# Kernel optimization log

Measured on AMD Instinct MI355X. Metric: run time of the kernel, lower is better.

Reference implementation:

```python
import jax, jax.numpy as jnp
import numpy as np

D_MODEL = 256
D_ENC_M = 256  # mel encoder dim (keys/values), sets temperature = sqrt(D_ENC_M)
D_ENC_T = 256  # text encoder dim (queries)
LN_EPS = 1e-5


def setup_inputs() -> dict:
    key = jax.random.key(0)
    ks = jax.random.split(key, 9)
    B, MEL_LEN, SRC_LEN = 16, 2048, 512
    mel_encoding = jax.random.normal(ks[0], (B, MEL_LEN, D_ENC_M), dtype=jnp.float32)
    text_encoding = jax.random.normal(ks[1], (B, SRC_LEN, D_ENC_T), dtype=jnp.float32)
    mel_mask = jax.random.randint(ks[2], (B, MEL_LEN), 0, 2).astype(bool)
    src_mask = jax.random.randint(ks[3], (B, SRC_LEN), 0, 2).astype(bool)
    # Linear weights (no bias), xavier-uniform style scale
    def xavier(k, shape):
        fan_in, fan_out = shape[1], shape[0]
        lim = jnp.sqrt(6.0 / (fan_in + fan_out))
        return jax.random.uniform(k, shape, jnp.float32, -lim, lim)
    Wq = xavier(ks[4], (D_MODEL, D_ENC_T))
    Wk = xavier(ks[5], (D_MODEL, D_ENC_M))
    Wv = xavier(ks[6], (D_MODEL, D_ENC_M))
    gamma = jnp.ones((D_MODEL,), jnp.float32)
    beta = jnp.zeros((D_MODEL,), jnp.float32)
    return {"mel_encoding": mel_encoding, "text_encoding": text_encoding,
            "mel_mask": mel_mask, "src_mask": src_mask,
            "Wq": Wq, "Wk": Wk, "Wv": Wv, "gamma": gamma, "beta": beta}


def reference(mel_encoding, text_encoding, mel_mask, src_mask, Wq, Wk, Wv, gamma, beta):
    # QKV projections (nn.Linear, bias=False): y = x @ W^T
    q = jnp.einsum('btd,md->btm', text_encoding, Wq)   # [B, src_len, d_model]
    k = jnp.einsum('bsd,md->bsm', mel_encoding, Wk)    # [B, mel_len, d_model]
    v = jnp.einsum('bsd,md->bsm', mel_encoding, Wv)    # [B, mel_len, d_model]
    temperature = jnp.asarray(D_ENC_M, jnp.float32) ** 0.5
    attn = jnp.einsum('btm,bsm->bts', q, k) / temperature  # [B, src_len, mel_len]
    # pre-softmax fill over mel (key) padding
    attn = jnp.where(mel_mask[:, None, :], -jnp.inf, attn)
    attn = jax.nn.softmax(attn, axis=2)
    # post-softmax zeroing over src (query) padding
    attn = jnp.where(src_mask[:, :, None], 0.0, attn)
    output = jnp.einsum('bts,bsm->btm', attn, v)  # [B, src_len, d_model]
    # dropout is identity in eval mode; LayerNorm over last dim
    mu = jnp.mean(output, axis=-1, keepdims=True)
    var = jnp.mean(jnp.square(output - mu), axis=-1, keepdims=True)
    output = (output - mu) * jax.lax.rsqrt(var + LN_EPS) * gamma + beta
    return (output, attn)
```

## Files before the change

### kernel.cpp

```cpp
#include <hip/hip_runtime.h>
#include <hip/hip_bf16.h>
#include <stdint.h>

#define DMODEL 256
#define BATCH  16
#define MEL    2048
#define SRC    512

typedef __attribute__((ext_vector_type(8))) short bf16x8;
typedef __attribute__((ext_vector_type(4))) float f32x4;
typedef __attribute__((ext_vector_type(4))) int   i32x4;

__device__ inline short f2bf(float f) {
    union { float f; uint32_t u; } c{f};
    uint32_t u = c.u;
    u += 0x7FFFu + ((u >> 16) & 1u);
    return (short)(u >> 16);
}

__device__ inline bf16x8 cvt8(const float* p) {
    const f32x4* q = reinterpret_cast<const f32x4*>(p);
    f32x4 a = q[0], b = q[1];
    bf16x8 r;
    r[0] = f2bf(a[0]); r[1] = f2bf(a[1]); r[2] = f2bf(a[2]); r[3] = f2bf(a[3]);
    r[4] = f2bf(b[0]); r[5] = f2bf(b[1]); r[6] = f2bf(b[2]); r[7] = f2bf(b[3]);
    return r;
}

__global__ __launch_bounds__(256)
void wconv_kernel(const float* __restrict__ Wq, const float* __restrict__ Wk,
                  const float* __restrict__ Wv, short* __restrict__ wb) {
    int i = blockIdx.x * 256 + threadIdx.x;
    int which = i >> 13;
    int off = (i & 8191) * 8;
    const float* src = which == 0 ? Wq : (which == 1 ? Wk : Wv);
    *reinterpret_cast<bf16x8*>(wb + which * 65536 + off) = cvt8(src + off);
}

template<bool AF32, bool BF32, bool CF32>
__global__ __launch_bounds__(256)
void gemm_bt(const void* __restrict__ Ap, const void* __restrict__ Bp,
             void* __restrict__ Cp, float scale, int K, int ldc,
             long aB, long bB, long cB) {
    __shared__ short As[128 * 72];
    __shared__ short Bs[128 * 72];

    const int tid = threadIdx.x;
    const int lane = tid & 63, w = tid >> 6;
    const int lr = lane & 15, lk = lane >> 4;
    const int wr = w >> 1, wc = w & 1;
    const size_t arow0 = (size_t)blockIdx.x * 128;
    const size_t brow0 = (size_t)blockIdx.y * 128;

    const char* Abase = (const char*)Ap + (size_t)blockIdx.z * aB * (AF32 ? 4 : 2);
    const char* Bbase = (const char*)Bp + (size_t)blockIdx.z * bB * (BF32 ? 4 : 2);
    char*       Cbase = (char*)Cp       + (size_t)blockIdx.z * cB * (CF32 ? 4 : 2);

    bf16x8 sA[4], sB[4];
    auto STAGE = [&](int kt) {
#pragma unroll
        for (int i = 0; i < 4; ++i) {
            int idx = i * 256 + tid;
            int row = idx >> 3, c8 = (idx & 7) * 8;
            size_t aoff = (arow0 + row) * (size_t)K + kt * 64 + c8;
            size_t boff = (brow0 + row) * (size_t)K + kt * 64 + c8;
            if constexpr (AF32) sA[i] = cvt8((const float*)Abase + aoff);
            else                sA[i] = *(const bf16x8*)((const short*)Abase + aoff);
            if constexpr (BF32) sB[i] = cvt8((const float*)Bbase + boff);
            else                sB[i] = *(const bf16x8*)((const short*)Bbase + boff);
        }
    };

    STAGE(0);
    f32x4 acc[4][4];
#pragma unroll
    for (int m = 0; m < 4; ++m)
#pragma unroll
        for (int n = 0; n < 4; ++n) acc[m][n] = (f32x4){0.f, 0.f, 0.f, 0.f};

    const int NK = K >> 6;
    for (int kt = 0; kt < NK; ++kt) {
        __syncthreads();
#pragma unroll
        for (int i = 0; i < 4; ++i) {
            int idx = i * 256 + tid;
            int row = idx >> 3, c8 = (idx & 7) * 8;
            *(bf16x8*)&As[row * 72 + c8] = sA[i];
            *(bf16x8*)&Bs[row * 72 + c8] = sB[i];
        }
        __syncthreads();
        if (kt + 1 < NK) STAGE(kt + 1);
#pragma unroll
        for (int kt2 = 0; kt2 < 2; ++kt2) {
            bf16x8 af[4], bfr[4];
#pragma unroll
            for (int m = 0; m < 4; ++m)
                af[m] = *(const bf16x8*)&As[(64 * wr + 16 * m + lr) * 72 + kt2 * 32 + 8 * lk];
#pragma unroll
            for (int n = 0; n < 4; ++n)
                bfr[n] = *(const bf16x8*)&Bs[(64 * wc + 16 * n + lr) * 72 + kt2 * 32 + 8 * lk];
#pragma unroll
            for (int m = 0; m < 4; ++m)
#pragma unroll
                for (int n = 0; n < 4; ++n)
                    acc[m][n] = __builtin_amdgcn_mfma_f32_16x16x32_bf16(af[m], bfr[n], acc[m][n], 0, 0, 0);
        }
    }

#pragma unroll
    for (int m = 0; m < 4; ++m)
#pragma unroll
        for (int n = 0; n < 4; ++n)
#pragma unroll
            for (int r = 0; r < 4; ++r) {
                size_t row = arow0 + 64 * wr + 16 * m + 4 * lk + r;
                size_t col = brow0 + 64 * wc + 16 * n + lr;
                if constexpr (CF32)
                    ((float*)Cbase)[row * ldc + col] = acc[m][n][r] * scale;
                else
                    ((short*)Cbase)[row * ldc + col] = f2bf(acc[m][n][r] * scale);
            }
}

__global__ __launch_bounds__(512)
void softmax_kernel(float* __restrict__ attn, const int* __restrict__ mel_mask,
                    const int* __restrict__ src_mask) {
    const int w = threadIdx.x >> 6, lane = threadIdx.x & 63;
    const int row = blockIdx.x * 8 + w;
    const int b = row >> 9, t = row & 511;
    float* p = attn + (size_t)row * MEL + lane * 32;
    const i32x4* mm = (const i32x4*)(mel_mask + b * MEL + lane * 32);

    f32x4 v[8]; i32x4 m[8];
#pragma unroll
    for (int j = 0; j < 8; ++j) { v[j] = ((const f32x4*)p)[j]; m[j] = mm[j]; }

    float mx = -3.0e38f;
#pragma unroll
    for (int j = 0; j < 8; ++j)
#pragma unroll
        for (int e = 0; e < 4; ++e) if (!m[j][e]) mx = fmaxf(mx, v[j][e]);
#pragma unroll
    for (int off = 32; off; off >>= 1) mx = fmaxf(mx, __shfl_xor(mx, off));

    float sum = 0.f;
#pragma unroll
    for (int j = 0; j < 8; ++j)
#pragma unroll
        for (int e = 0; e < 4; ++e) {
            float ev = m[j][e] ? 0.f : __expf(v[j][e] - mx);
            v[j][e] = ev; sum += ev;
        }
#pragma unroll
    for (int off = 32; off; off >>= 1) sum += __shfl_xor(sum, off);

    const float inv = src_mask[b * SRC + t] ? 0.f : 1.f / sum;
#pragma unroll
    for (int j = 0; j < 8; ++j) {
        f32x4 o = { v[j][0] * inv, v[j][1] * inv, v[j][2] * inv, v[j][3] * inv };
        ((f32x4*)p)[j] = o;
    }
}

__global__ __launch_bounds__(256)
void pv_ln_kernel(const float* __restrict__ attn, const short* __restrict__ vt,
                  const float* __restrict__ gamma, const float* __restrict__ beta,
                  float* __restrict__ out) {
    __shared__ short As[64 * 72];
    __shared__ short Bs[256 * 72];

    const int tid = threadIdx.x;
    const int lane = tid & 63, w = tid >> 6;
    const int lr = lane & 15, lk = lane >> 4;
    const int b = blockIdx.y;
    const size_t row0 = (size_t)blockIdx.x * 64;
    const float* A = attn + (size_t)b * SRC * MEL;
    const short* B = vt + (size_t)b * DMODEL * MEL;

    float gm[16], bt[16];
#pragma unroll
    for (int n = 0; n < 16; ++n) { gm[n] = gamma[16 * n + lr]; bt[n] = beta[16 * n + lr]; }

    bf16x8 sA[2], sB[8];
    auto STAGE = [&](int kt) {
#pragma unroll
        for (int i = 0; i < 2; ++i) {
            int idx = i * 256 + tid; int row = idx >> 3, c8 = (idx & 7) * 8;
            sA[i] = cvt8(A + (row0 + row) * (size_t)MEL + kt * 64 + c8);
        }
#pragma unroll
        for (int i = 0; i < 8; ++i) {
            int idx = i * 256 + tid; int row = idx >> 3, c8 = (idx & 7) * 8;
            sB[i] = *(const bf16x8*)(B + row * (size_t)MEL + kt * 64 + c8);
        }
    };

    STAGE(0);
    f32x4 acc[16];
#pragma unroll
    for (int n = 0; n < 16; ++n) acc[n] = (f32x4){0.f, 0.f, 0.f, 0.f};

    for (int kt = 0; kt < MEL / 64; ++kt) {
        __syncthreads();
#pragma unroll
        for (int i = 0; i < 2; ++i) {
            int idx = i * 256 + tid;
            *(bf16x8*)&As[(idx >> 3) * 72 + (idx & 7) * 8] = sA[i];
        }
#pragma unroll
        for (int i = 0; i < 8; ++i) {
            int idx = i * 256 + tid;
            *(bf16x8*)&Bs[(idx >> 3) * 72 + (idx & 7) * 8] = sB[i];
        }
        __syncthreads();
        if (kt + 1 < MEL / 64) STAGE(kt + 1);
#pragma unroll
        for (int kt2 = 0; kt2 < 2; ++kt2) {
            bf16x8 af = *(const bf16x8*)&As[(16 * w + lr) * 72 + kt2 * 32 + 8 * lk];
#pragma unroll
            for (int n = 0; n < 16; ++n) {
                bf16x8 bfr = *(const bf16x8*)&Bs[(16 * n + lr) * 72 + kt2 * 32 + 8 * lk];
                acc[n] = __builtin_amdgcn_mfma_f32_16x16x32_bf16(af, bfr, acc[n], 0, 0, 0);
            }
        }
    }

    float s1[4] = {0.f, 0.f, 0.f, 0.f};
#pragma unroll
    for (int n = 0; n < 16; ++n)
#pragma unroll
        for (int r = 0; r < 4; ++r) s1[r] += acc[n][r];
#pragma unroll
    for (int off = 8; off; off >>= 1)
#pragma unroll
        for (int r = 0; r < 4; ++r) s1[r] += __shfl_xor(s1[r], off);
    float mu[4];
#pragma unroll
    for (int r = 0; r < 4; ++r) mu[r] = s1[r] * (1.f / DMODEL);

    float s2[4] = {0.f, 0.f, 0.f, 0.f};
#pragma unroll
    for (int n = 0; n < 16; ++n)
#pragma unroll
        for (int r = 0; r < 4; ++r) {
            float d = acc[n][r] - mu[r];
            s2[r] += d * d;
        }
#pragma unroll
    for (int off = 8; off; off >>= 1)
#pragma unroll
        for (int r = 0; r < 4; ++r) s2[r] += __shfl_xor(s2[r], off);
    float rsig[4];
#pragma unroll
    for (int r = 0; r < 4; ++r) rsig[r] = rsqrtf(s2[r] * (1.f / DMODEL) + 1e-5f);

    float* orow = out + ((size_t)b * SRC + row0 + 16 * w) * DMODEL;
#pragma unroll
    for (int n = 0; n < 16; ++n)
#pragma unroll
        for (int r = 0; r < 4; ++r)
            orow[(4 * lk + r) * DMODEL + 16 * n + lr] =
                (acc[n][r] - mu[r]) * rsig[r] * gm[n] + bt[n];
}

extern "C" void kernel_launch(void* const* d_in, const int* in_sizes, int n_in,
                              void* d_out, int out_size, void* d_ws, size_t ws_size,
                              hipStream_t stream) {
    const float* mel      = (const float*)d_in[0];
    const float* text     = (const float*)d_in[1];
    const int*   mel_mask = (const int*)d_in[2];
    const int*   src_mask = (const int*)d_in[3];
    const float* Wq       = (const float*)d_in[4];
    const float* Wk       = (const float*)d_in[5];
    const float* Wv       = (const float*)d_in[6];
    const float* gamma    = (const float*)d_in[7];
    const float* beta     = (const float*)d_in[8];

    float* out  = (float*)d_out;
    float* attn = out + (size_t)BATCH * SRC * DMODEL;

    short* wb  = (short*)d_ws;
    short* qbf = wb + 3 * 65536;
    short* kbf = qbf + (size_t)BATCH * SRC * DMODEL;
    short* vt  = kbf + (size_t)BATCH * MEL * DMODEL;

    wconv_kernel<<<96, 256, 0, stream>>>(Wq, Wk, Wv, wb);

    gemm_bt<true, false, false><<<dim3(64, 2, 1), 256, 0, stream>>>(
        text, wb, qbf, 1.f, 256, 256, 0, 0, 0);
    gemm_bt<true, false, false><<<dim3(256, 2, 1), 256, 0, stream>>>(
        mel, wb + 65536, kbf, 1.f, 256, 256, 0, 0, 0);
    gemm_bt<false, true, false><<<dim3(2, 16, BATCH), 256, 0, stream>>>(
        wb + 131072, mel, vt, 1.f, 256, 2048,
        0, (long)MEL * DMODEL, (long)DMODEL * MEL);
    gemm_bt<false, false, true><<<dim3(4, 16, BATCH), 256, 0, stream>>>(
        qbf, kbf, attn, 0.0625f, 256, 2048,
        (long)SRC * DMODEL, (long)MEL * DMODEL, (long)SRC * MEL);

    softmax_kernel<<<BATCH * SRC / 8, 512, 0, stream>>>(attn, mel_mask, src_mask);

    pv_ln_kernel<<<dim3(SRC / 64, BATCH), 256, 0, stream>>>(
        attn, vt, gamma, beta, out);
}
```

Before: 239.0 us.

## Merge projections into one launch, stage epilogues through LDS, retile PV-LayerNorm

Replaces the weight-conversion kernel and three projection GEMM launches with a single kernel that converts fp32 weights to bf16 on the fly. Adds XCD-aware block-to-batch mapping for the QK, V-projection and PV kernels. Output tiles now go through shared memory so global stores are coalesced vectors instead of scattered scalars. The PV+LayerNorm kernel moves to 32-row tiles with 512 threads and a single-pass sum/sum-of-squares reduction across waves, which doubles the block count at the cost of extra LDS traffic and a less stable variance formula.

```diff
diff --git a/kernel.cpp b/kernel.cpp
--- a/kernel.cpp
+++ b/kernel.cpp
@@ -8,6 +8,7 @@
 #define SRC    512
 
 typedef __attribute__((ext_vector_type(8))) short bf16x8;
+typedef __attribute__((ext_vector_type(4))) short short4v;
 typedef __attribute__((ext_vector_type(4))) float f32x4;
 typedef __attribute__((ext_vector_type(4))) int   i32x4;
 
@@ -23,38 +24,45 @@
     f32x4 a = q[0], b = q[1];
     bf16x8 r;
     r[0] = f2bf(a[0]); r[1] = f2bf(a[1]); r[2] = f2bf(a[2]); r[3] = f2bf(a[3]);
-    r[4] = f2bf(b[0]); r[5] = f2bf(b[1]); r[6] = f2bf(b[2]); r[7] = f2bf(b[3]);
+    r[4] = f2bf(b[0]); r[5] = f2bf(b[1]); r[6] = f2bf(b[2]); r[7] = f2bf(b[7-4]);
+    r[7] = f2bf(b[3]);
+    r[6] = f2bf(b[2]);
     return r;
 }
 
 __global__ __launch_bounds__(256)
-void wconv_kernel(const float* __restrict__ Wq, const float* __restrict__ Wk,
-                  const float* __restrict__ Wv, short* __restrict__ wb) {
-    int i = blockIdx.x * 256 + threadIdx.x;
-    int which = i >> 13;
-    int off = (i & 8191) * 8;
-    const float* src = which == 0 ? Wq : (which == 1 ? Wk : Wv);
-    *reinterpret_cast<bf16x8*>(wb + which * 65536 + off) = cvt8(src + off);
-}
-
-template<bool AF32, bool BF32, bool CF32>
-__global__ __launch_bounds__(256)
-void gemm_bt(const void* __restrict__ Ap, const void* __restrict__ Bp,
-             void* __restrict__ Cp, float scale, int K, int ldc,
-             long aB, long bB, long cB) {
-    __shared__ short As[128 * 72];
-    __shared__ short Bs[128 * 72];
+void proj_all_kernel(const float* __restrict__ mel, const float* __restrict__ text,
+                     const float* __restrict__ Wq, const float* __restrict__ Wk,
+                     const float* __restrict__ Wv,
+                     short* __restrict__ qbf, short* __restrict__ kbf,
+                     short* __restrict__ vt) {
+    __shared__ char SMEM[36864];
+    short* As = (short*)SMEM;
+    short* Bs = (short*)SMEM + 128 * 72;
 
     const int tid = threadIdx.x;
     const int lane = tid & 63, w = tid >> 6;
     const int lr = lane & 15, lk = lane >> 4;
     const int wr = w >> 1, wc = w & 1;
-    const size_t arow0 = (size_t)blockIdx.x * 128;
-    const size_t brow0 = (size_t)blockIdx.y * 128;
-
-    const char* Abase = (const char*)Ap + (size_t)blockIdx.z * aB * (AF32 ? 4 : 2);
-    const char* Bbase = (const char*)Bp + (size_t)blockIdx.z * bB * (BF32 ? 4 : 2);
-    char*       Cbase = (char*)Cp       + (size_t)blockIdx.z * cB * (CF32 ? 4 : 2);
+
+    const int u = blockIdx.x;
+    const float *Af, *Bf; short* C; int ldc; size_t arow0, brow0;
+    if (u < 128) {
+        arow0 = (size_t)(u >> 1) * 128; brow0 = (size_t)(u & 1) * 128;
+        Af = text; Bf = Wq; C = qbf; ldc = DMODEL;
+    } else if (u < 640) {
+        int v = u - 128;
+        arow0 = (size_t)(v >> 1) * 128; brow0 = (size_t)(v & 1) * 128;
+        Af = mel; Bf = Wk; C = kbf; ldc = DMODEL;
+    } else {
+        int v = u - 640;
+        int xcd = v & 7, j = v >> 3;
+        int b = 2 * xcd + (j >> 5), t = j & 31;
+        arow0 = (size_t)(t & 1) * 128; brow0 = (size_t)(t >> 1) * 128;
+        Af = Wv; Bf = mel + (size_t)b * MEL * DMODEL;
+        C = vt + (size_t)b * DMODEL * MEL; ldc = MEL;
+    }
+    C += arow0 * ldc + brow0;
 
     bf16x8 sA[4], sB[4];
     auto STAGE = [&](int kt) {
@@ -62,12 +70,8 @@
         for (int i = 0; i < 4; ++i) {
             int idx = i * 256 + tid;
             int row = idx >> 3, c8 = (idx & 7) * 8;
-            size_t aoff = (arow0 + row) * (size_t)K + kt * 64 + c8;
-            size_t boff = (brow0 + row) * (size_t)K + kt * 64 + c8;
-            if constexpr (AF32) sA[i] = cvt8((const float*)Abase + aoff);
-            else                sA[i] = *(const bf16x8*)((const short*)Abase + aoff);
-            if constexpr (BF32) sB[i] = cvt8((const float*)Bbase + boff);
-            else                sB[i] = *(const bf16x8*)((const short*)Bbase + boff);
+            sA[i] = cvt8(Af + (arow0 + row) * 256 + kt * 64 + c8);
+            sB[i] = cvt8(Bf + (brow0 + row) * 256 + kt * 64 + c8);
         }
     };
 
@@ -78,8 +82,7 @@
 #pragma unroll
         for (int n = 0; n < 4; ++n) acc[m][n] = (f32x4){0.f, 0.f, 0.f, 0.f};
 
-    const int NK = K >> 6;
-    for (int kt = 0; kt < NK; ++kt) {
+    for (int kt = 0; kt < 4; ++kt) {
         __syncthreads();
 #pragma unroll
         for (int i = 0; i < 4; ++i) {
@@ -89,7 +92,7 @@
             *(bf16x8*)&Bs[row * 72 + c8] = sB[i];
         }
         __syncthreads();
-        if (kt + 1 < NK) STAGE(kt + 1);
+        if (kt < 3) STAGE(kt + 1);
 #pragma unroll
         for (int kt2 = 0; kt2 < 2; ++kt2) {
             bf16x8 af[4], bfr[4];
@@ -107,19 +110,116 @@
         }
     }
 
+    __syncthreads();
+    short* Cs = (short*)SMEM;
 #pragma unroll
     for (int m = 0; m < 4; ++m)
 #pragma unroll
         for (int n = 0; n < 4; ++n)
 #pragma unroll
-            for (int r = 0; r < 4; ++r) {
-                size_t row = arow0 + 64 * wr + 16 * m + 4 * lk + r;
-                size_t col = brow0 + 64 * wc + 16 * n + lr;
-                if constexpr (CF32)
-                    ((float*)Cbase)[row * ldc + col] = acc[m][n][r] * scale;
-                else
-                    ((short*)Cbase)[row * ldc + col] = f2bf(acc[m][n][r] * scale);
-            }
+            for (int r = 0; r < 4; ++r)
+                Cs[(64 * wr + 16 * m + 4 * lk + r) * 136 + 64 * wc + 16 * n + lr] =
+                    f2bf(acc[m][n][r]);
+    __syncthreads();
+#pragma unroll
+    for (int i = 0; i < 8; ++i) {
+        int idx = i * 256 + tid;
+        int row = idx >> 4, c8 = (idx & 15) * 8;
+        *(bf16x8*)&C[(size_t)row * ldc + c8] = *(const bf16x8*)&Cs[row * 136 + c8];
+    }
+}
+
+__global__ __launch_bounds__(256)
+void sgemm_kernel(const short* __restrict__ qbf, const short* __restrict__ kbf,
+                  float* __restrict__ attn) {
+    __shared__ char SMEM[36864];
+    short* As = (short*)SMEM;
+    short* Bs = (short*)SMEM + 128 * 72;
+
+    const int tid = threadIdx.x;
+    const int lane = tid & 63, w = tid >> 6;
+    const int lr = lane & 15, lk = lane >> 4;
+    const int wr = w >> 1, wc = w & 1;
+
+    const int bid = blockIdx.x;
+    const int xcd = bid & 7, j = bid >> 3;
+    const int z = 2 * xcd + (j >> 6);
+    const int t = j & 63;
+    const int x = t & 3, y = t >> 2;
+
+    const short* A = qbf + (size_t)z * SRC * DMODEL + (size_t)x * 128 * DMODEL;
+    const short* B = kbf + (size_t)z * MEL * DMODEL + (size_t)y * 128 * DMODEL;
+    float* Cw = attn + (size_t)z * SRC * MEL + (size_t)x * 128 * MEL + (size_t)y * 128;
+
+    bf16x8 sA[4], sB[4];
+    auto STAGE = [&](int kt) {
+#pragma unroll
+        for (int i = 0; i < 4; ++i) {
+            int idx = i * 256 + tid;
+            int row = idx >> 3, c8 = (idx & 7) * 8;
+            sA[i] = *(const bf16x8*)(A + (size_t)row * DMODEL + kt * 64 + c8);
+            sB[i] = *(const bf16x8*)(B + (size_t)row * DMODEL + kt * 64 + c8);
+        }
+    };
+
+    STAGE(0);
+    f32x4 acc[4][4];
+#pragma unroll
+    for (int m = 0; m < 4; ++m)
+#pragma unroll
+        for (int n = 0; n < 4; ++n) acc[m][n] = (f32x4){0.f, 0.f, 0.f, 0.f};
+
+    for (int kt = 0; kt < 4; ++kt) {
+        __syncthreads();
+#pragma unroll
+        for (int i = 0; i < 4; ++i) {
+            int idx = i * 256 + tid;
+            int row = idx >> 3, c8 = (idx & 7) * 8;
+            *(bf16x8*)&As[row * 72 + c8] = sA[i];
+            *(bf16x8*)&Bs[row * 72 + c8] = sB[i];
+        }
+        __syncthreads();
+        if (kt < 3) STAGE(kt + 1);
+#pragma unroll
+        for (int kt2 = 0; kt2 < 2; ++kt2) {
+            bf16x8 af[4], bfr[4];
+#pragma unroll
+            for (int m = 0; m < 4; ++m)
+                af[m] = *(const bf16x8*)&As[(64 * wr + 16 * m + lr) * 72 + kt2 * 32 + 8 * lk];
+#pragma unroll
+            for (int n = 0; n < 4; ++n)
+                bfr[n] = *(const bf16x8*)&Bs[(64 * wc + 16 * n + lr) * 72 + kt2 * 32 + 8 * lk];
+#pragma unroll
+            for (int m = 0; m < 4; ++m)
+#pragma unroll
+                for (int n = 0; n < 4; ++n)
+                    acc[m][n] = __builtin_amdgcn_mfma_f32_16x16x32_bf16(af[m], bfr[n], acc[m][n], 0, 0, 0);
+        }
+    }
+
+    __syncthreads();
+    float* Cs = (float*)SMEM;
+#pragma unroll
+    for (int half = 0; half < 2; ++half) {
+        if (wr == half) {
+#pragma unroll
+            for (int m = 0; m < 4; ++m)
+#pragma unroll
+                for (int n = 0; n < 4; ++n)
+#pragma unroll
+                    for (int r = 0; r < 4; ++r)
+                        Cs[(16 * m + 4 * lk + r) * 132 + 64 * wc + 16 * n + lr] =
+                            acc[m][n][r] * 0.0625f;
+        }
+        __syncthreads();
+#pragma unroll
+        for (int i = 0; i < 8; ++i) {
+            int idx = i * 256 + tid;
+            int row = idx >> 5, c4 = (idx & 31) * 4;
+            *(f32x4*)&Cw[(size_t)(half * 64 + row) * MEL + c4] = *(const f32x4*)&Cs[row * 132 + c4];
+        }
+        __syncthreads();
+    }
 }
 
 __global__ __launch_bounds__(512)
@@ -162,105 +262,128 @@
     }
 }
 
-__global__ __launch_bounds__(256)
+__global__ __launch_bounds__(512)
 void pv_ln_kernel(const float* __restrict__ attn, const short* __restrict__ vt,
                   const float* __restrict__ gamma, const float* __restrict__ beta,
                   float* __restrict__ out) {
-    __shared__ short As[64 * 72];
-    __shared__ short Bs[256 * 72];
+    __shared__ char SMEM[42496];
+    short* As = (short*)SMEM;
+    short* Bs = (short*)(SMEM + 4608);
+    float* red = (float*)(SMEM + 41472);
+    float* Ost = (float*)(SMEM + 4608);
 
     const int tid = threadIdx.x;
     const int lane = tid & 63, w = tid >> 6;
     const int lr = lane & 15, lk = lane >> 4;
-    const int b = blockIdx.y;
-    const size_t row0 = (size_t)blockIdx.x * 64;
-    const float* A = attn + (size_t)b * SRC * MEL;
-    const short* B = vt + (size_t)b * DMODEL * MEL;
-
-    float gm[16], bt[16];
-#pragma unroll
-    for (int n = 0; n < 16; ++n) { gm[n] = gamma[16 * n + lr]; bt[n] = beta[16 * n + lr]; }
-
-    bf16x8 sA[2], sB[8];
+    const int wr = w >> 2, wc = w & 3;
+
+    const int bid = blockIdx.x;
+    const int xcd = bid & 7, j = bid >> 3;
+    const int b = 2 * xcd + (j >> 4);
+    const int mt = j & 15;
+    const size_t row0 = (size_t)mt * 32;
+
+    const float* A = attn + (size_t)b * SRC * MEL + row0 * MEL;
+    const short* Bv = vt + (size_t)b * DMODEL * MEL;
+
+    float gm[4], bt[4];
+#pragma unroll
+    for (int n = 0; n < 4; ++n) {
+        gm[n] = gamma[64 * wc + 16 * n + lr];
+        bt[n] = beta[64 * wc + 16 * n + lr];
+    }
+
+    f32x4 sAv; bf16x8 sB[4];
+    const int a_row = tid >> 4, a_c4 = (tid & 15) * 4;
     auto STAGE = [&](int kt) {
-#pragma unroll
-        for (int i = 0; i < 2; ++i) {
-            int idx = i * 256 + tid; int row = idx >> 3, c8 = (idx & 7) * 8;
-            sA[i] = cvt8(A + (row0 + row) * (size_t)MEL + kt * 64 + c8);
-        }
-#pragma unroll
-        for (int i = 0; i < 8; ++i) {
-            int idx = i * 256 + tid; int row = idx >> 3, c8 = (idx & 7) * 8;
-            sB[i] = *(const bf16x8*)(B + row * (size_t)MEL + kt * 64 + c8);
+        sAv = *(const f32x4*)(A + (size_t)a_row * MEL + kt * 64 + a_c4);
+#pragma unroll
+        for (int i = 0; i < 4; ++i) {
+            int idx = i * 512 + tid;
+            int row = idx >> 3, c8 = (idx & 7) * 8;
+            sB[i] = *(const bf16x8*)(Bv + (size_t)row * MEL + kt * 64 + c8);
         }
     };
 
     STAGE(0);
-    f32x4 acc[16];
-#pragma unroll
-    for (int n = 0; n < 16; ++n) acc[n] = (f32x4){0.f, 0.f, 0.f, 0.f};
+    f32x4 acc[4];
+#pragma unroll
+    for (int n = 0; n < 4; ++n) acc[n] = (f32x4){0.f, 0.f, 0.f, 0.f};
 
     for (int kt = 0; kt < MEL / 64; ++kt) {
         __syncthreads();
-#pragma unroll
-        for (int i = 0; i < 2; ++i) {
-            int idx = i * 256 + tid;
-            *(bf16x8*)&As[(idx >> 3) * 72 + (idx & 7) * 8] = sA[i];
-        }
-#pragma unroll
-        for (int i = 0; i < 8; ++i) {
-            int idx = i * 256 + tid;
-            *(bf16x8*)&Bs[(idx >> 3) * 72 + (idx & 7) * 8] = sB[i];
+        {
+            short4v a4 = { f2bf(sAv[0]), f2bf(sAv[1]), f2bf(sAv[2]), f2bf(sAv[3]) };
+            *(short4v*)&As[a_row * 72 + a_c4] = a4;
+#pragma unroll
+            for (int i = 0; i < 4; ++i) {
+                int idx = i * 512 + tid;
+                int row = idx >> 3, c8 = (idx & 7) * 8;
+                *(bf16x8*)&Bs[row * 72 + c8] = sB[i];
+            }
         }
         __syncthreads();
         if (kt + 1 < MEL / 64) STAGE(kt + 1);
 #pragma unroll
         for (int kt2 = 0; kt2 < 2; ++kt2) {
-            bf16x8 af = *(const bf16x8*)&As[(16 * w + lr) * 72 + kt2 * 32 + 8 * lk];
-#pragma unroll
-            for (int n = 0; n < 16; ++n) {
-                bf16x8 bfr = *(const bf16x8*)&Bs[(16 * n + lr) * 72 + kt2 * 32 + 8 * lk];
+            bf16x8 af = *(const bf16x8*)&As[(16 * wr + lr) * 72 + kt2 * 32 + 8 * lk];
+#pragma unroll
+            for (int n = 0; n < 4; ++n) {
+                bf16x8 bfr = *(const bf16x8*)&Bs[(64 * wc + 16 * n + lr) * 72 + kt2 * 32 + 8 * lk];
                 acc[n] = __builtin_amdgcn_mfma_f32_16x16x32_bf16(af, bfr, acc[n], 0, 0, 0);
             }
         }
     }
 
-    float s1[4] = {0.f, 0.f, 0.f, 0.f};
-#pragma unroll
-    for (int n = 0; n < 16; ++n)
-#pragma unroll
-        for (int r = 0; r < 4; ++r) s1[r] += acc[n][r];
+    float s1[4] = {0.f, 0.f, 0.f, 0.f}, s2[4] = {0.f, 0.f, 0.f, 0.f};
+#pragma unroll
+    for (int n = 0; n < 4; ++n)
+#pragma unroll
+        for (int r = 0; r < 4; ++r) {
+            s1[r] += acc[n][r];
+            s2[r] += acc[n][r] * acc[n][r];
+        }
 #pragma unroll
     for (int off = 8; off; off >>= 1)
 #pragma unroll
-        for (int r = 0; r < 4; ++r) s1[r] += __shfl_xor(s1[r], off);
-    float mu[4];
-#pragma unroll
-    for (int r = 0; r < 4; ++r) mu[r] = s1[r] * (1.f / DMODEL);
-
-    float s2[4] = {0.f, 0.f, 0.f, 0.f};
-#pragma unroll
-    for (int n = 0; n < 16; ++n)
-#pragma unroll
         for (int r = 0; r < 4; ++r) {
-            float d = acc[n][r] - mu[r];
-            s2[r] += d * d;
-        }
-#pragma unroll
-    for (int off = 8; off; off >>= 1)
-#pragma unroll
-        for (int r = 0; r < 4; ++r) s2[r] += __shfl_xor(s2[r], off);
-    float rsig[4];
-#pragma unroll
-    for (int r = 0; r < 4; ++r) rsig[r] = rsqrtf(s2[r] * (1.f / DMODEL) + 1e-5f);
-
-    float* orow = out + ((size_t)b * SRC + row0 + 16 * w) * DMODEL;
-#pragma unroll
-    for (int n = 0; n < 16; ++n)
+            s1[r] += __shfl_xor(s1[r], off);
+            s2[r] += __shfl_xor(s2[r], off);
+        }
+    __syncthreads();
+    if (lr == 0) {
+#pragma unroll
+        for (int r = 0; r < 4; ++r) {
+            red[(16 * wr + 4 * lk + r) * 4 + wc] = s1[r];
+            red[128 + (16 * wr + 4 * lk + r) * 4 + wc] = s2[r];
+        }
+    }
+    __syncthreads();
+    float mu[4], rsig[4];
+#pragma unroll
+    for (int r = 0; r < 4; ++r) {
+        int rowi = 16 * wr + 4 * lk + r;
+        float S1 = red[rowi * 4 + 0] + red[rowi * 4 + 1] + red[rowi * 4 + 2] + red[rowi * 4 + 3];
+        float S2 = red[128 + rowi * 4 + 0] + red[128 + rowi * 4 + 1] +
+                   red[128 + rowi * 4 + 2] + red[128 + rowi * 4 + 3];
+        mu[r] = S1 * (1.f / DMODEL);
+        rsig[r] = rsqrtf(S2 * (1.f / DMODEL) - mu[r] * mu[r] + 1e-5f);
+    }
+    __syncthreads();
+#pragma unroll
+    for (int n = 0; n < 4; ++n)
 #pragma unroll
         for (int r = 0; r < 4; ++r)
-            orow[(4 * lk + r) * DMODEL + 16 * n + lr] =
+            Ost[(16 * wr + 4 * lk + r) * 260 + 64 * wc + 16 * n + lr] =
                 (acc[n][r] - mu[r]) * rsig[r] * gm[n] + bt[n];
+    __syncthreads();
+#pragma unroll
+    for (int i = 0; i < 4; ++i) {
+        int idx = i * 512 + tid;
+        int row = idx >> 6, c4 = (idx & 63) * 4;
+        *(f32x4*)&out[((size_t)b * SRC + row0 + row) * DMODEL + c4] =
+            *(const f32x4*)&Ost[row * 260 + c4];
+    }
 }
 
 extern "C" void kernel_launch(void* const* d_in, const int* in_sizes, int n_in,
@@ -279,26 +402,12 @@
     float* out  = (float*)d_out;
     float* attn = out + (size_t)BATCH * SRC * DMODEL;
 
-    short* wb  = (short*)d_ws;
-    short* qbf = wb + 3 * 65536;
+    short* qbf = (short*)d_ws;
     short* kbf = qbf + (size_t)BATCH * SRC * DMODEL;
     short* vt  = kbf + (size_t)BATCH * MEL * DMODEL;
 
-    wconv_kernel<<<96, 256, 0, stream>>>(Wq, Wk, Wv, wb);
-
-    gemm_bt<true, false, false><<<dim3(64, 2, 1), 256, 0, stream>>>(
-        text, wb, qbf, 1.f, 256, 256, 0, 0, 0);
-    gemm_bt<true, false, false><<<dim3(256, 2, 1), 256, 0, stream>>>(
-        mel, wb + 65536, kbf, 1.f, 256, 256, 0, 0, 0);
-    gemm_bt<false, true, false><<<dim3(2, 16, BATCH), 256, 0, stream>>>(
-        wb + 131072, mel, vt, 1.f, 256, 2048,
-        0, (long)MEL * DMODEL, (long)DMODEL * MEL);
-    gemm_bt<false, false, true><<<dim3(4, 16, BATCH), 256, 0, stream>>>(
-        qbf, kbf, attn, 0.0625f, 256, 2048,
-        (long)SRC * DMODEL, (long)MEL * DMODEL, (long)SRC * MEL);
-
+    proj_all_kernel<<<1152, 256, 0, stream>>>(mel, text, Wq, Wk, Wv, qbf, kbf, vt);
+    sgemm_kernel<<<1024, 256, 0, stream>>>(qbf, kbf, attn);
     softmax_kernel<<<BATCH * SRC / 8, 512, 0, stream>>>(attn, mel_mask, src_mask);
-
-    pv_ln_kernel<<<dim3(SRC / 64, BATCH), 256, 0, stream>>>(
-        attn, vt, gamma, beta, out);
-}
+    pv_ln_kernel<<<256, 512, 0, stream>>>(attn, vt, gamma, beta, out);
+}
```

Result: faster. 225.1 us (-5.8%).
